# Kernel tuning notes

Hardware: AMD Instinct MI355X
Metric: run time of the kernel (lower is better)

The kernel has to match this reference:

```python
import jax, jax.numpy as jnp
import numpy as np

B, T, D, E = 2, 1653, 512, 8
D_E = D // E
BE = B * E


def setup_inputs() -> dict:
    key = jax.random.key(0)
    ks = jax.random.split(key, 11)
    s = 0.02  # keep linear-layer scale sane
    return {
        "input": jax.random.normal(ks[0], (B, T, D), jnp.float32),
        "Wq": jax.random.normal(ks[1], (D, D), jnp.float32) * s,
        "bq": jax.random.normal(ks[2], (D,), jnp.float32) * s,
        "Wk": jax.random.normal(ks[3], (D, D), jnp.float32) * s,
        "bk": jax.random.normal(ks[4], (D,), jnp.float32) * s,
        "Wv": jax.random.normal(ks[5], (D, D), jnp.float32) * s,
        "bv": jax.random.normal(ks[6], (D,), jnp.float32) * s,
        "Wo": jax.random.normal(ks[7], (D, D), jnp.float32) * s,
        "bo": jax.random.normal(ks[8], (D,), jnp.float32) * s,
        # random 'gaussian orthogonal punishment' matrix (diag(norms) @ blockwise-QR in torch; random here)
        "punish": jax.random.normal(ks[9], (T, T), jnp.float32) * (1.0 / np.sqrt(T)),
        # random tensor produced by torch.nn.init.orthogonal_(att_score) in the source
        "att_orth": jax.random.normal(ks[10], (BE, T, T), jnp.float32) * (1.0 / np.sqrt(T)),
    }


def _learnable_sigmoid(x):
    return 1.2 / (1.0 + jnp.exp(-1.6 * x))


def reference(input, Wq, bq, Wk, bk, Wv, bv, Wo, bo, punish, att_orth):
    # torch nn.Linear: y = x @ W^T + b
    def proj(W, b):
        # [B,T,D] -> permute(0,2,1) -> [B,D,T] -> reshape to [B*E, T, D_E]
        y = jnp.einsum('btd,ed->bte', input, W) + b
        return y.transpose(0, 2, 1).reshape(BE, T, D_E)

    Q = _learnable_sigmoid(proj(Wq, bq))            # [BE, T, D_E] (mask_q is all-ones => no-op)
    K = _learnable_sigmoid(proj(Wk, bk))            # [BE, T, D_E]
    V = proj(Wv, bv)                                # [BE, T, D_E]

    inv_sqrt_T = 1.0 / jnp.sqrt(jnp.float32(T))
    att = jnp.einsum('btd,bsd->bts', Q, K) * inv_sqrt_T  # [BE, T, T]

    # punishment: elementwise mul by broadcast punish matrix, then matmul with
    # the (transposed) random orthogonal tensor: att = (att * P) @ orth^T
    att = (att * punish[None, :, :]) @ att_orth.transpose(0, 2, 1)  # [BE, T, T]

    att = jnp.where(att == 0.0, jnp.float32(-2e20), att)  # masked_fill(att==0, -2e20)

    out = jnp.einsum('bts,bsd->btd', att, V)        # [BE, T, D_E]
    # permute(0,2,1) -> [BE, D_E, T] -> reshape [B, D, T] -> permute -> [B, T, D]
    out = out.transpose(0, 2, 1).reshape(B, D, T).transpose(0, 2, 1)
    return jnp.einsum('btd,ed->bte', out, Wo) + bo   # [B, T, D]
```

## Files before the change

kernel.cpp:

```cpp
#include <hip/hip_runtime.h>

#define TT 1653
#define DD 512
#define BB 2
#define DE 64
#define BEH 16
#define TTILES 26
#define TPAD 1664
#define STILE 128
#define SQN 13
#define NJC 4
#define MPSTRIDE TPAD

typedef __attribute__((ext_vector_type(8))) short bf16x8;
typedef __attribute__((ext_vector_type(4))) float f32x4;
typedef short bf16x8u __attribute__((ext_vector_type(8), aligned(4)));

__device__ __forceinline__ short f2bf(float f) {
    union { float f; unsigned u; } v; v.f = f;
    unsigned r = v.u + 0x7fffu + ((v.u >> 16) & 1u);
    return (short)(r >> 16);
}
__device__ __forceinline__ unsigned pack2(float a, float b) {
    return (unsigned)(unsigned short)f2bf(a) | ((unsigned)(unsigned short)f2bf(b) << 16);
}
__device__ __forceinline__ float bf2f(short s) {
    union { unsigned u; float f; } v; v.u = ((unsigned)(unsigned short)s) << 16;
    return v.f;
}
__device__ __forceinline__ bf16x8 ld_frag4(const short* p) {
    bf16x8u v = *(const bf16x8u*)p;
    return (bf16x8)v;
}

__global__ __launch_bounds__(256) void convp2_kernel(
    const float* __restrict__ P, short* __restrict__ Pbf)
{
    const int g = blockIdx.x * 256 + threadIdx.x;
    const int NG4 = TPAD / 4;
    if (g >= TT * NG4) return;
    const int r = g / NG4, c4 = (g - r * NG4) * 4;
    float p0 = 0.f, p1 = 0.f, p2 = 0.f, p3 = 0.f;
    const float* prow = P + (size_t)r * TT;
    if (c4 + 0 < TT) p0 = prow[c4 + 0];
    if (c4 + 1 < TT) p1 = prow[c4 + 1];
    if (c4 + 2 < TT) p2 = prow[c4 + 2];
    if (c4 + 3 < TT) p3 = prow[c4 + 3];
    uint2 o; o.x = pack2(p0, p1); o.y = pack2(p2, p3);
    *(uint2*)(Pbf + (size_t)r * TPAD + c4) = o;
}

__global__ __launch_bounds__(256) void proj2_kernel(
    const float* __restrict__ X,
    const float* __restrict__ W0, const float* __restrict__ b0,
    const float* __restrict__ W1, const float* __restrict__ b1,
    const float* __restrict__ W2, const float* __restrict__ b2,
    short* __restrict__ Y0, short* __restrict__ Y1, short* __restrict__ Y2)
{
    __shared__ short Wsh[64][72];
    __shared__ short Xs[64][72];

    const int tt = blockIdx.x, dt = blockIdx.y, z = blockIdx.z;
    const int b = z / 3, which = z % 3;
    const float* W    = (which == 0) ? W0 : (which == 1) ? W1 : W2;
    const float* bias = (which == 0) ? b0 : (which == 1) ? b1 : b2;
    short* Y          = (which == 0) ? Y0 : (which == 1) ? Y1 : Y2;

    const int t0 = tt * 64, d0 = dt * 64;
    const float* Xb = X + (size_t)b * TT * DD;

    const int tid  = threadIdx.x;
    const int wave = tid >> 6, lane = tid & 63;
    const int quad = lane >> 4, l16 = lane & 15;
    const int srow = tid >> 2, scg = (tid & 3) * 16;

    f32x4 acc[4];
    #pragma unroll
    for (int i = 0; i < 4; ++i) acc[i] = (f32x4){0.f, 0.f, 0.f, 0.f};

    for (int k0 = 0; k0 < DD; k0 += 64) {
        {
            const float* wrow = W + (size_t)(d0 + srow) * DD + k0 + scg;
            float4 w0 = *(const float4*)(wrow);
            float4 w1 = *(const float4*)(wrow + 4);
            float4 w2 = *(const float4*)(wrow + 8);
            float4 w3 = *(const float4*)(wrow + 12);
            uint4 pw0, pw1;
            pw0.x = pack2(w0.x, w0.y); pw0.y = pack2(w0.z, w0.w);
            pw0.z = pack2(w1.x, w1.y); pw0.w = pack2(w1.z, w1.w);
            pw1.x = pack2(w2.x, w2.y); pw1.y = pack2(w2.z, w2.w);
            pw1.z = pack2(w3.x, w3.y); pw1.w = pack2(w3.z, w3.w);

            const int t = t0 + srow;
            float4 x0 = make_float4(0.f,0.f,0.f,0.f), x1 = x0, x2 = x0, x3 = x0;
            if (t < TT) {
                const float* xrow = Xb + (size_t)t * DD + k0 + scg;
                x0 = *(const float4*)(xrow);
                x1 = *(const float4*)(xrow + 4);
                x2 = *(const float4*)(xrow + 8);
                x3 = *(const float4*)(xrow + 12);
            }
            uint4 px0, px1;
            px0.x = pack2(x0.x, x0.y); px0.y = pack2(x0.z, x0.w);
            px0.z = pack2(x1.x, x1.y); px0.w = pack2(x1.z, x1.w);
            px1.x = pack2(x2.x, x2.y); px1.y = pack2(x2.z, x2.w);
            px1.z = pack2(x3.x, x3.y); px1.w = pack2(x3.z, x3.w);

            __syncthreads();
            *(uint4*)&Wsh[srow][scg]     = pw0;
            *(uint4*)&Wsh[srow][scg + 8] = pw1;
            *(uint4*)&Xs[srow][scg]      = px0;
            *(uint4*)&Xs[srow][scg + 8]  = px1;
        }
        __syncthreads();

        #pragma unroll
        for (int ks = 0; ks < 2; ++ks) {
            bf16x8 a = *(const bf16x8*)&Wsh[wave * 16 + l16][ks * 32 + quad * 8];
            #pragma unroll
            for (int nt = 0; nt < 4; ++nt) {
                bf16x8 bb = *(const bf16x8*)&Xs[nt * 16 + l16][ks * 32 + quad * 8];
                acc[nt] = __builtin_amdgcn_mfma_f32_16x16x32_bf16(a, bb, acc[nt], 0, 0, 0);
            }
        }
    }

    #pragma unroll
    for (int nt = 0; nt < 4; ++nt) {
        const int t = t0 + nt * 16 + l16;
        if (t < TT) {
            #pragma unroll
            for (int r = 0; r < 4; ++r) {
                const int d = d0 + wave * 16 + quad * 4 + r;
                float v = acc[nt][r] + bias[d];
                if (which < 2) v = 1.2f / (1.0f + __expf(-1.6f * v));
                Y[((size_t)b * DD + d) * TT + t] = f2bf(v);
            }
        }
    }
}

__global__ __launch_bounds__(256) void ovt3_kernel(
    const float* __restrict__ orth, const short* __restrict__ Vb,
    float* __restrict__ Mpart)
{
    __shared__ short Os[STILE][66];
    __shared__ short Vs[64][66];

    const int sq = blockIdx.x, be = blockIdx.y, jc = blockIdx.z;
    const int s0 = sq * STILE;
    const int jt0 = (jc < 2) ? jc * 7 : 14 + (jc - 2) * 6;
    const int jtn = (jc < 2) ? 7 : 6;

    const float* O  = orth + (size_t)be * TT * TT;
    const short* Vh = Vb + (size_t)be * DE * TT;

    const int tid  = threadIdx.x;
    const int wave = tid >> 6, lane = tid & 63;
    const int quad = lane >> 4, l16 = lane & 15;

    f32x4 acc[4][2];
    #pragma unroll
    for (int i = 0; i < 4; ++i)
        #pragma unroll
        for (int j = 0; j < 2; ++j) acc[i][j] = (f32x4){0.f, 0.f, 0.f, 0.f};

    for (int t = 0; t < jtn; ++t) {
        const int j0 = (jt0 + t) * 64;

        #pragma unroll
        for (int u = 0; u < 8; ++u) {
            const int jl = wave * 16 + 2 * u;
            const int j  = j0 + jl;

            float o0[2] = {0.f, 0.f}, o1[2] = {0.f, 0.f};
            #pragma unroll
            for (int i = 0; i < 2; ++i) {
                const int c = s0 + lane + 64 * i;
                if (c < TT) {
                    if (j < TT)     o0[i] = O[(size_t)j * TT + c];
                    if (j + 1 < TT) o1[i] = O[(size_t)(j + 1) * TT + c];
                }
            }
            #pragma unroll
            for (int i = 0; i < 2; ++i)
                *(unsigned*)&Os[lane + 64 * i][jl] = pack2(o0[i], o1[i]);

            short v0 = 0, v1 = 0;
            if (j < TT)     v0 = Vh[(size_t)j * DE + lane];
            if (j + 1 < TT) v1 = Vh[(size_t)(j + 1) * DE + lane];
            *(unsigned*)&Vs[lane][jl] =
                (unsigned)(unsigned short)v0 | ((unsigned)(unsigned short)v1 << 16);
        }
        __syncthreads();

        #pragma unroll
        for (int ks = 0; ks < 2; ++ks) {
            bf16x8 a[4], bb[2];
            #pragma unroll
            for (int i = 0; i < 4; ++i)
                a[i] = ld_frag4(&Vs[i * 16 + l16][ks * 32 + quad * 8]);
            #pragma unroll
            for (int jj = 0; jj < 2; ++jj)
                bb[jj] = ld_frag4(&Os[wave * 32 + jj * 16 + l16][ks * 32 + quad * 8]);
            #pragma unroll
            for (int i = 0; i < 4; ++i)
                #pragma unroll
                for (int jj = 0; jj < 2; ++jj)
                    acc[i][jj] = __builtin_amdgcn_mfma_f32_16x16x32_bf16(a[i], bb[jj], acc[i][jj], 0, 0, 0);
        }
        __syncthreads();
    }

    float* Mp = Mpart + (size_t)(jc * BEH + be) * DE * MPSTRIDE;
    #pragma unroll
    for (int i = 0; i < 4; ++i) {
        #pragma unroll
        for (int jj = 0; jj < 2; ++jj) {
            const int s = s0 + wave * 32 + jj * 16 + l16;
            #pragma unroll
            for (int r = 0; r < 4; ++r) {
                const int d = i * 16 + quad * 4 + r;
                Mp[(size_t)d * MPSTRIDE + s] = acc[i][jj][r];
            }
        }
    }
}

__global__ __launch_bounds__(256) void mreduce_kernel(
    const float* __restrict__ Mpart, short* __restrict__ Mt)
{
    const int g = blockIdx.x * 256 + threadIdx.x;
    const int NG = TPAD / 4;
    if (g >= BEH * DE * NG) return;
    const int bd = g / NG;
    const int s4 = (g - bd * NG) * 4;

    const size_t jstride = (size_t)BEH * DE * MPSTRIDE;
    const float* p = Mpart + (size_t)bd * MPSTRIDE + s4;
    float4 a0 = *(const float4*)(p);
    float4 a1 = *(const float4*)(p + jstride);
    float4 a2 = *(const float4*)(p + 2 * jstride);
    float4 a3 = *(const float4*)(p + 3 * jstride);
    float s0 = a0.x + a1.x + a2.x + a3.x;
    float s1 = a0.y + a1.y + a2.y + a3.y;
    float s2 = a0.z + a1.z + a2.z + a3.z;
    float s3 = a0.w + a1.w + a2.w + a3.w;

    uint2 o;
    o.x = pack2(s0, s1);
    o.y = pack2(s2, s3);
    *(uint2*)(Mt + (size_t)bd * TPAD + s4) = o;
}

__global__ __launch_bounds__(256) void attn2_kernel(
    const short* __restrict__ Qb, const short* __restrict__ Kb,
    const short* __restrict__ Mt, const short* __restrict__ Pbf,
    float* __restrict__ Hbuf)
{
    __shared__ short Qs[64][72];
    __shared__ short Ks[64][72];
    __shared__ short Ms[64][72];
    __shared__ short Wl[64][72];
    __shared__ short Ps[64][72];

    const int it = blockIdx.x, be = blockIdx.y;
    const int b = be >> 3, e = be & 7;
    const int i0 = it * 64;
    const short* Qh = Qb + (size_t)be * DE * TT;
    const short* Kh = Kb + (size_t)be * DE * TT;
    const short* Mh = Mt + (size_t)be * DE * TPAD;

    const int tid  = threadIdx.x;
    const int wave = tid >> 6, lane = tid & 63;
    const int quad = lane >> 4, l16 = lane & 15;

    const float invs = 0.024598297f;

    const int srow = tid >> 2, scg = (tid & 3) * 16;

    {
        const int gi = i0 + srow;
        uint4 z = make_uint4(0u, 0u, 0u, 0u);
        uint4 v0 = z, v1 = z;
        if (gi < TT) {
            v0 = *(const uint4*)(Qh + (size_t)gi * DE + scg);
            v1 = *(const uint4*)(Qh + (size_t)gi * DE + scg + 8);
        }
        *(uint4*)&Qs[srow][scg]     = v0;
        *(uint4*)&Qs[srow][scg + 8] = v1;
    }

    f32x4 out[4];
    #pragma unroll
    for (int i = 0; i < 4; ++i) out[i] = (f32x4){0.f, 0.f, 0.f, 0.f};

    for (int s0 = 0; s0 < TT; s0 += 64) {
        {
            const int gs = s0 + srow;
            uint4 z = make_uint4(0u, 0u, 0u, 0u);
            uint4 k0 = z, k1 = z;
            if (gs < TT) {
                k0 = *(const uint4*)(Kh + (size_t)gs * DE + scg);
                k1 = *(const uint4*)(Kh + (size_t)gs * DE + scg + 8);
            }
            *(uint4*)&Ks[srow][scg]     = k0;
            *(uint4*)&Ks[srow][scg + 8] = k1;

            uint4 m0 = *(const uint4*)(Mh + (size_t)srow * TPAD + s0 + scg);
            uint4 m1 = *(const uint4*)(Mh + (size_t)srow * TPAD + s0 + scg + 8);
            *(uint4*)&Ms[srow][scg]     = m0;
            *(uint4*)&Ms[srow][scg + 8] = m1;

            const int gi = i0 + srow;
            uint4 p0 = z, p1 = z;
            if (gi < TT) {
                p0 = *(const uint4*)(Pbf + (size_t)gi * TPAD + s0 + scg);
                p1 = *(const uint4*)(Pbf + (size_t)gi * TPAD + s0 + scg + 8);
            }
            *(uint4*)&Ps[srow][scg]     = p0;
            *(uint4*)&Ps[srow][scg + 8] = p1;
        }
        __syncthreads();

        f32x4 w[4];
        #pragma unroll
        for (int i = 0; i < 4; ++i) w[i] = (f32x4){0.f, 0.f, 0.f, 0.f};
        #pragma unroll
        for (int ks = 0; ks < 2; ++ks) {
            bf16x8 a = *(const bf16x8*)&Qs[wave * 16 + l16][ks * 32 + quad * 8];
            #pragma unroll
            for (int stile = 0; stile < 4; ++stile) {
                bf16x8 bb = *(const bf16x8*)&Ks[stile * 16 + l16][ks * 32 + quad * 8];
                w[stile] = __builtin_amdgcn_mfma_f32_16x16x32_bf16(a, bb, w[stile], 0, 0, 0);
            }
        }

        #pragma unroll
        for (int stile = 0; stile < 4; ++stile) {
            const int sl = stile * 16 + l16;
            #pragma unroll
            for (int r = 0; r < 4; ++r) {
                const int il = wave * 16 + quad * 4 + r;
                float v = w[stile][r] * invs * bf2f(Ps[il][sl]);
                Wl[il][sl] = f2bf(v);
            }
        }

        #pragma unroll
        for (int ks = 0; ks < 2; ++ks) {
            bf16x8 a = *(const bf16x8*)&Wl[wave * 16 + l16][ks * 32 + quad * 8];
            #pragma unroll
            for (int dt = 0; dt < 4; ++dt) {
                bf16x8 bb = *(const bf16x8*)&Ms[dt * 16 + l16][ks * 32 + quad * 8];
                out[dt] = __builtin_amdgcn_mfma_f32_16x16x32_bf16(a, bb, out[dt], 0, 0, 0);
            }
        }
        __syncthreads();
    }

    #pragma unroll
    for (int dt = 0; dt < 4; ++dt) {
        const int d = dt * 16 + l16;
        #pragma unroll
        for (int r = 0; r < 4; ++r) {
            const int gi = i0 + wave * 16 + quad * 4 + r;
            if (gi < TT)
                Hbuf[((size_t)b * TT + gi) * DD + e * 64 + d] = out[dt][r];
        }
    }
}

__global__ __launch_bounds__(256) void oproj_kernel(
    const float* __restrict__ H, const float* __restrict__ Wo,
    const float* __restrict__ bo, float* __restrict__ out)
{
    __shared__ float Hs[16][68];
    __shared__ float Ns[16][68];

    const int tt = blockIdx.x, nt = blockIdx.y, b = blockIdx.z;
    const int t0 = tt * 64, n0 = nt * 64;
    const float* Hb = H + (size_t)b * TT * DD;

    const int tid = threadIdx.x;
    const int tx = tid & 15, ty = tid >> 4;
    const int lrow = tid >> 2, lq = tid & 3;
    const int trow = t0 + lrow;

    float acc[4][4] = {};

    for (int k0 = 0; k0 < DD; k0 += 16) {
        float4 hv = make_float4(0.f, 0.f, 0.f, 0.f);
        if (trow < TT)
            hv = *(const float4*)(Hb + (size_t)trow * DD + k0 + lq*4);
        float4 wv = *(const float4*)(Wo + (size_t)(n0 + lrow) * DD + k0 + lq*4);
        __syncthreads();
        Hs[lq*4+0][lrow] = hv.x; Hs[lq*4+1][lrow] = hv.y;
        Hs[lq*4+2][lrow] = hv.z; Hs[lq*4+3][lrow] = hv.w;
        Ns[lq*4+0][lrow] = wv.x; Ns[lq*4+1][lrow] = wv.y;
        Ns[lq*4+2][lrow] = wv.z; Ns[lq*4+3][lrow] = wv.w;
        __syncthreads();
        #pragma unroll
        for (int k = 0; k < 16; ++k) {
            float4 a4 = *(const float4*)(&Hs[k][ty*4]);
            float4 c4 = *(const float4*)(&Ns[k][tx*4]);
            float a[4] = {a4.x, a4.y, a4.z, a4.w};
            float c[4] = {c4.x, c4.y, c4.z, c4.w};
            #pragma unroll
            for (int i = 0; i < 4; ++i)
                #pragma unroll
                for (int j = 0; j < 4; ++j)
                    acc[i][j] = fmaf(a[i], c[j], acc[i][j]);
        }
        __syncthreads();
    }

    #pragma unroll
    for (int i = 0; i < 4; ++i) {
        const int t = t0 + ty*4 + i;
        if (t < TT) {
            float4 v;
            v.x = acc[i][0] + bo[n0 + tx*4 + 0];
            v.y = acc[i][1] + bo[n0 + tx*4 + 1];
            v.z = acc[i][2] + bo[n0 + tx*4 + 2];
            v.w = acc[i][3] + bo[n0 + tx*4 + 3];
            *(float4*)(out + ((size_t)b * TT + t) * DD + n0 + tx*4) = v;
        }
    }
}

extern "C" void kernel_launch(void* const* d_in, const int* in_sizes, int n_in,
                              void* d_out, int out_size, void* d_ws, size_t ws_size,
                              hipStream_t stream)
{
    (void)in_sizes; (void)n_in; (void)out_size; (void)ws_size;

    const float* X    = (const float*)d_in[0];
    const float* Wq   = (const float*)d_in[1];
    const float* bq   = (const float*)d_in[2];
    const float* Wk   = (const float*)d_in[3];
    const float* bk   = (const float*)d_in[4];
    const float* Wv   = (const float*)d_in[5];
    const float* bv   = (const float*)d_in[6];
    const float* Wo   = (const float*)d_in[7];
    const float* bo   = (const float*)d_in[8];
    const float* P    = (const float*)d_in[9];
    const float* orth = (const float*)d_in[10];
    float* out = (float*)d_out;

    char* ws = (char*)d_ws;
    const size_t SZH = (size_t)BB * DD * TT * sizeof(short);
    short* Qb  = (short*)(ws);
    short* Kb  = (short*)(ws + SZH);
    short* Vb  = (short*)(ws + 2 * SZH);
    short* Mtb = (short*)(ws + 3 * SZH);
    short* Pbf = (short*)(ws + 3 * SZH + (size_t)BEH * DE * TPAD * sizeof(short));
    char*  after_p = ws + 3 * SZH + (size_t)BEH * DE * TPAD * sizeof(short)
                        + (size_t)TT * TPAD * sizeof(short);
    float* Mpart = (float*)after_p;
    float* Hbuf  = (float*)after_p;

    dim3 blk(256);

    convp2_kernel<<<dim3((TT * (TPAD / 4) + 255) / 256), blk, 0, stream>>>(P, Pbf);

    dim3 g1(TTILES, DD / 64, BB * 3);
    proj2_kernel<<<g1, blk, 0, stream>>>(X, Wq, bq, Wk, bk, Wv, bv, Qb, Kb, Vb);

    dim3 g2(SQN, BEH, NJC);
    ovt3_kernel<<<g2, blk, 0, stream>>>(orth, Vb, Mpart);

    dim3 gr((BEH * DE * (TPAD / 4) + 255) / 256);
    mreduce_kernel<<<gr, blk, 0, stream>>>(Mpart, Mtb);

    dim3 g3(TTILES, BEH);
    attn2_kernel<<<g3, blk, 0, stream>>>(Qb, Kb, Mtb, Pbf, Hbuf);

    dim3 g4(TTILES, DD / 64, BB);
    oproj_kernel<<<g4, blk, 0, stream>>>(Hbuf, Wo, bo, out);
}
```

Before: 425.6 us.

## Vectorize and prefetch orth/V loads in OV kernel with smaller S tiles

Rewrites the orth·V partial-product kernel so it uses 64-wide S tiles, doubling the grid, and sets launch bounds for higher occupancy. Global reads of the fp32 orth matrix and the V rows become 16-byte and 8-byte vector loads instead of scalar ones. The next tile is register-prefetched while the current tile is consumed, so global latency overlaps with the MFMA work. In exchange, each block does half the MFMA work per LDS fill, and the transpose-pack writes into shared memory may see more bank conflicts.

After: 409.4 us. 3.8% less time.

```diff
diff --git a/kernel.cpp b/kernel.cpp
--- a/kernel.cpp
+++ b/kernel.cpp
@@ -7,14 +7,14 @@
 #define BEH 16
 #define TTILES 26
 #define TPAD 1664
-#define STILE 128
-#define SQN 13
+#define SQN 26
 #define NJC 4
 #define MPSTRIDE TPAD
 
 typedef __attribute__((ext_vector_type(8))) short bf16x8;
 typedef __attribute__((ext_vector_type(4))) float f32x4;
 typedef short bf16x8u __attribute__((ext_vector_type(8), aligned(4)));
+typedef float f32x4u  __attribute__((ext_vector_type(4), aligned(4)));
 
 __device__ __forceinline__ short f2bf(float f) {
     union { float f; unsigned u; } v; v.f = f;
@@ -140,15 +140,15 @@
     }
 }
 
-__global__ __launch_bounds__(256) void ovt3_kernel(
+__global__ __launch_bounds__(256, 6) void ovt4_kernel(
     const float* __restrict__ orth, const short* __restrict__ Vb,
     float* __restrict__ Mpart)
 {
-    __shared__ short Os[STILE][66];
+    __shared__ short Os[64][66];
     __shared__ short Vs[64][66];
 
     const int sq = blockIdx.x, be = blockIdx.y, jc = blockIdx.z;
-    const int s0 = sq * STILE;
+    const int s0 = sq * 64;
     const int jt0 = (jc < 2) ? jc * 7 : 14 + (jc - 2) * 6;
     const int jtn = (jc < 2) ? 7 : 6;
 
@@ -159,70 +159,89 @@
     const int wave = tid >> 6, lane = tid & 63;
     const int quad = lane >> 4, l16 = lane & 15;
 
-    f32x4 acc[4][2];
-    #pragma unroll
-    for (int i = 0; i < 4; ++i)
-        #pragma unroll
-        for (int j = 0; j < 2; ++j) acc[i][j] = (f32x4){0.f, 0.f, 0.f, 0.f};
-
+    const int c4 = tid & 15;
+    const int pr = tid >> 4;
+    const int ca = s0 + 4 * c4;
+    const bool fastS = (s0 + 64 <= TT);
+
+    f32x4 acc[4];
+    #pragma unroll
+    for (int i = 0; i < 4; ++i) acc[i] = (f32x4){0.f, 0.f, 0.f, 0.f};
+
+    f32x4u o0a, o0b, o1a, o1b;
+    uint2  v0a, v0b, v1a, v1b;
+
+    auto stage_load = [&](int j0) {
+        const int jA0 = j0 + 2 * pr;
+        const int jA1 = jA0 + 32;
+        const int r0  = min(jA0,     TT - 1);
+        const int r0b = min(jA0 + 1, TT - 1);
+        const int r1  = min(jA1,     TT - 1);
+        const int r1b = min(jA1 + 1, TT - 1);
+        if (fastS) {
+            o0a = *(const f32x4u*)(O + (size_t)r0  * TT + ca);
+            o0b = *(const f32x4u*)(O + (size_t)r0b * TT + ca);
+            o1a = *(const f32x4u*)(O + (size_t)r1  * TT + ca);
+            o1b = *(const f32x4u*)(O + (size_t)r1b * TT + ca);
+        } else {
+            #pragma unroll
+            for (int i = 0; i < 4; ++i) {
+                const int col = ca + i;
+                const bool cv = (col < TT);
+                o0a[i] = cv ? O[(size_t)r0  * TT + col] : 0.f;
+                o0b[i] = cv ? O[(size_t)r0b * TT + col] : 0.f;
+                o1a[i] = cv ? O[(size_t)r1  * TT + col] : 0.f;
+                o1b[i] = cv ? O[(size_t)r1b * TT + col] : 0.f;
+            }
+        }
+        const uint2 z = make_uint2(0u, 0u);
+        v0a = (jA0     < TT) ? *(const uint2*)(Vh + (size_t)jA0       * DE + 4 * c4) : z;
+        v0b = (jA0 + 1 < TT) ? *(const uint2*)(Vh + (size_t)(jA0 + 1) * DE + 4 * c4) : z;
+        v1a = (jA1     < TT) ? *(const uint2*)(Vh + (size_t)jA1       * DE + 4 * c4) : z;
+        v1b = (jA1 + 1 < TT) ? *(const uint2*)(Vh + (size_t)(jA1 + 1) * DE + 4 * c4) : z;
+    };
+
+    auto lds_write = [&]() {
+        #pragma unroll
+        for (int i = 0; i < 4; ++i) {
+            *(unsigned*)&Os[4 * c4 + i][2 * pr]      = pack2(o0a[i], o0b[i]);
+            *(unsigned*)&Os[4 * c4 + i][2 * pr + 32] = pack2(o1a[i], o1b[i]);
+        }
+        *(unsigned*)&Vs[4 * c4 + 0][2 * pr]      = (v0a.x & 0xffffu) | (v0b.x << 16);
+        *(unsigned*)&Vs[4 * c4 + 1][2 * pr]      = (v0a.x >> 16)     | (v0b.x & 0xffff0000u);
+        *(unsigned*)&Vs[4 * c4 + 2][2 * pr]      = (v0a.y & 0xffffu) | (v0b.y << 16);
+        *(unsigned*)&Vs[4 * c4 + 3][2 * pr]      = (v0a.y >> 16)     | (v0b.y & 0xffff0000u);
+        *(unsigned*)&Vs[4 * c4 + 0][2 * pr + 32] = (v1a.x & 0xffffu) | (v1b.x << 16);
+        *(unsigned*)&Vs[4 * c4 + 1][2 * pr + 32] = (v1a.x >> 16)     | (v1b.x & 0xffff0000u);
+        *(unsigned*)&Vs[4 * c4 + 2][2 * pr + 32] = (v1a.y & 0xffffu) | (v1b.y << 16);
+        *(unsigned*)&Vs[4 * c4 + 3][2 * pr + 32] = (v1a.y >> 16)     | (v1b.y & 0xffff0000u);
+    };
+
+    stage_load(jt0 * 64);
     for (int t = 0; t < jtn; ++t) {
-        const int j0 = (jt0 + t) * 64;
-
-        #pragma unroll
-        for (int u = 0; u < 8; ++u) {
-            const int jl = wave * 16 + 2 * u;
-            const int j  = j0 + jl;
-
-            float o0[2] = {0.f, 0.f}, o1[2] = {0.f, 0.f};
-            #pragma unroll
-            for (int i = 0; i < 2; ++i) {
-                const int c = s0 + lane + 64 * i;
-                if (c < TT) {
-                    if (j < TT)     o0[i] = O[(size_t)j * TT + c];
-                    if (j + 1 < TT) o1[i] = O[(size_t)(j + 1) * TT + c];
-                }
-            }
-            #pragma unroll
-            for (int i = 0; i < 2; ++i)
-                *(unsigned*)&Os[lane + 64 * i][jl] = pack2(o0[i], o1[i]);
-
-            short v0 = 0, v1 = 0;
-            if (j < TT)     v0 = Vh[(size_t)j * DE + lane];
-            if (j + 1 < TT) v1 = Vh[(size_t)(j + 1) * DE + lane];
-            *(unsigned*)&Vs[lane][jl] =
-                (unsigned)(unsigned short)v0 | ((unsigned)(unsigned short)v1 << 16);
-        }
-        __syncthreads();
-
+        if (t) __syncthreads();
+        lds_write();
+        if (t + 1 < jtn) stage_load((jt0 + t + 1) * 64);
+        __syncthreads();
         #pragma unroll
         for (int ks = 0; ks < 2; ++ks) {
-            bf16x8 a[4], bb[2];
-            #pragma unroll
-            for (int i = 0; i < 4; ++i)
-                a[i] = ld_frag4(&Vs[i * 16 + l16][ks * 32 + quad * 8]);
-            #pragma unroll
-            for (int jj = 0; jj < 2; ++jj)
-                bb[jj] = ld_frag4(&Os[wave * 32 + jj * 16 + l16][ks * 32 + quad * 8]);
-            #pragma unroll
-            for (int i = 0; i < 4; ++i)
-                #pragma unroll
-                for (int jj = 0; jj < 2; ++jj)
-                    acc[i][jj] = __builtin_amdgcn_mfma_f32_16x16x32_bf16(a[i], bb[jj], acc[i][jj], 0, 0, 0);
-        }
-        __syncthreads();
+            bf16x8 bb = ld_frag4(&Os[wave * 16 + l16][ks * 32 + quad * 8]);
+            #pragma unroll
+            for (int i = 0; i < 4; ++i) {
+                bf16x8 a = ld_frag4(&Vs[i * 16 + l16][ks * 32 + quad * 8]);
+                acc[i] = __builtin_amdgcn_mfma_f32_16x16x32_bf16(a, bb, acc[i], 0, 0, 0);
+            }
+        }
     }
 
     float* Mp = Mpart + (size_t)(jc * BEH + be) * DE * MPSTRIDE;
+    const int s = s0 + wave * 16 + l16;
     #pragma unroll
     for (int i = 0; i < 4; ++i) {
         #pragma unroll
-        for (int jj = 0; jj < 2; ++jj) {
-            const int s = s0 + wave * 32 + jj * 16 + l16;
-            #pragma unroll
-            for (int r = 0; r < 4; ++r) {
-                const int d = i * 16 + quad * 4 + r;
-                Mp[(size_t)d * MPSTRIDE + s] = acc[i][jj][r];
-            }
+        for (int r = 0; r < 4; ++r) {
+            const int d = i * 16 + quad * 4 + r;
+            Mp[(size_t)d * MPSTRIDE + s] = acc[i][r];
         }
     }
 }
@@ -468,7 +487,7 @@
     proj2_kernel<<<g1, blk, 0, stream>>>(X, Wq, bq, Wk, bk, Wv, bv, Qb, Kb, Vb);
 
     dim3 g2(SQN, BEH, NJC);
-    ovt3_kernel<<<g2, blk, 0, stream>>>(orth, Vb, Mpart);
+    ovt4_kernel<<<g2, blk, 0, stream>>>(orth, Vb, Mpart);
 
     dim3 gr((BEH * DE * (TPAD / 4) + 255) / 256);
     mreduce_kernel<<<gr, blk, 0, stream>>>(Mpart, Mtb);
```
